# Performance work log

Measured on AMD Instinct MI355X. Metric: run time of the kernel, lower is better.

The kernel has to match this reference:

```python
import jax, jax.numpy as jnp
import numpy as np

NEG_SLOPE = 0.2


def _gat_layer(x, W, a_src, a_dst, src, dst, ew, num_nodes):
    # Dense projection: [N, Din] @ [Din, Dout] -> [N, Dout]
    h = x @ W
    s = h @ a_src  # per-node source score, [N]
    d = h @ a_dst  # per-node destination score, [N]
    score = jax.nn.leaky_relu(s[src] + d[dst], NEG_SLOPE)  # [E]
    # segment softmax over incoming edges of each destination node
    m = jax.ops.segment_max(score, dst, num_segments=num_nodes)
    ex = jnp.exp(score - m[dst])
    denom = jax.ops.segment_sum(ex, dst, num_segments=num_nodes)
    alpha = ex / jnp.maximum(denom[dst], jnp.asarray(1e-16, ex.dtype))
    alpha = alpha * ew  # edge-weighted attention
    # gather h_j, scale by alpha, scatter-add into destinations
    return jax.ops.segment_sum(h[src] * alpha[:, None], dst, num_segments=num_nodes)


def setup_inputs() -> dict:
    key = jax.random.key(0)
    ks = jax.random.split(key, 9)
    N, E, F_IN, HID, NC = 100000, 1600000, 256, 64, 40
    x = jax.random.normal(ks[0], (N, F_IN), dtype=jnp.float32)
    edge_index = jax.random.randint(ks[1], (2, E), 0, N, dtype=jnp.int32)
    edge_weight = jax.random.uniform(ks[2], (E,), dtype=jnp.float32)
    W1 = jax.random.normal(ks[3], (F_IN, HID), dtype=jnp.float32) / np.sqrt(F_IN)
    a1_src = jax.random.normal(ks[4], (HID,), dtype=jnp.float32) / np.sqrt(HID)
    a1_dst = jax.random.normal(ks[5], (HID,), dtype=jnp.float32) / np.sqrt(HID)
    W2 = jax.random.normal(ks[6], (HID, NC), dtype=jnp.float32) / np.sqrt(HID)
    a2_src = jax.random.normal(ks[7], (NC,), dtype=jnp.float32) / np.sqrt(NC)
    a2_dst = jax.random.normal(ks[8], (NC,), dtype=jnp.float32) / np.sqrt(NC)
    return {"x": x, "edge_index": edge_index, "edge_weight": edge_weight,
            "W1": W1, "a1_src": a1_src, "a1_dst": a1_dst,
            "W2": W2, "a2_src": a2_src, "a2_dst": a2_dst}


def reference(x, edge_index, edge_weight, W1, a1_src, a1_dst, W2, a2_src, a2_dst):
    N = x.shape[0]
    # add_self_loops=True in both convs: append (i, i) edges with weight 1
    loops = jnp.arange(N, dtype=edge_index.dtype)
    src = jnp.concatenate([edge_index[0], loops])
    dst = jnp.concatenate([edge_index[1], loops])
    ew = jnp.concatenate([edge_weight, jnp.ones((N,), edge_weight.dtype)])
    h = jax.nn.relu(_gat_layer(x, W1, a1_src, a1_dst, src, dst, ew, N))
    # dropout inactive in eval mode
    out = _gat_layer(h, W2, a2_src, a2_dst, src, dst, ew, N)
    return out
```

## Files before the change

### kernel.cpp

```cpp
#include <hip/hip_runtime.h>
#include <hip/hip_bf16.h>
#include <math.h>

#define NEG_SLOPE 0.2f

typedef __attribute__((ext_vector_type(4))) float f32x4;
typedef __attribute__((ext_vector_type(8))) short bf16x8;
typedef __attribute__((ext_vector_type(4))) short bf16x4;

__device__ __forceinline__ float leaky(float x) { return x > 0.f ? x : NEG_SLOPE * x; }

__device__ __forceinline__ unsigned short bf_hi(float x) {
  return (unsigned short)(__float_as_uint(x) >> 16);
}

__device__ __forceinline__ unsigned short bf_rne(float x) {
  unsigned u = __float_as_uint(x);
  return (unsigned short)((u + 0x7FFFu + ((u >> 16) & 1u)) >> 16);
}


#define BIN_CHUNK 2048
#define BCAP 8192

__global__ void k_curinit(int* __restrict__ cursor, int NB) {
  int i = blockIdx.x * blockDim.x + threadIdx.x;
  if (i < NB) cursor[i] = i * BCAP;
}

__global__ __launch_bounds__(256)
void k_bin(const int* __restrict__ ei, const float* __restrict__ ew, int E, int N,
           int* __restrict__ cursor, int2* __restrict__ staged, int NB) {
  __shared__ int lhist[512];
  __shared__ int lbase[512];
  int tid = threadIdx.x;
  int start = blockIdx.x * BIN_CHUNK;
  int NT = E + N;
  int srcv[8], dstv[8]; float wv[8];
#pragma unroll
  for (int j = 0; j < 8; j++) {
    int e = start + j * 256 + tid;
    int s = 0, d = -1; float w = 0.f;
    if (e < NT) {
      if (e < E) { s = ei[e]; d = ei[E + e]; w = ew[e]; }
      else       { s = d = e - E; w = 1.f; }
    }
    srcv[j] = s; dstv[j] = d; wv[j] = w;
  }
  for (int b = tid; b < NB; b += 256) lhist[b] = 0;
  __syncthreads();
#pragma unroll
  for (int j = 0; j < 8; j++)
    if (dstv[j] >= 0) atomicAdd(&lhist[dstv[j] >> 8], 1);
  __syncthreads();
  for (int b = tid; b < NB; b += 256) {
    int n = lhist[b];
    lbase[b] = (n > 0) ? atomicAdd(&cursor[b], n) : 0;
    lhist[b] = 0;
  }
  __syncthreads();
#pragma unroll
  for (int j = 0; j < 8; j++) {
    if (dstv[j] >= 0) {
      int bkt = dstv[j] >> 8;
      int off = atomicAdd(&lhist[bkt], 1);
      staged[lbase[bkt] + off] =
          make_int2(srcv[j] | ((dstv[j] & 255) << 24), __float_as_int(wv[j]));
    }
  }
}

__global__ __launch_bounds__(512)
void k_bscan(const int* __restrict__ cursor, int NB, int NT, int N,
             int* __restrict__ bbase, int* __restrict__ rp) {
  __shared__ int sm[512];
  int tid = threadIdx.x;
  int v = (tid < NB) ? cursor[tid] - tid * BCAP : 0;
  sm[tid] = v;
  __syncthreads();
  for (int off = 1; off < 512; off <<= 1) {
    int x = sm[tid];
    int a = (tid >= off) ? sm[tid - off] : 0;
    __syncthreads();
    sm[tid] = x + a;
    __syncthreads();
  }
  if (tid < NB) bbase[tid] = sm[tid] - v;
  if (tid == 0) { bbase[NB] = sm[NB - 1]; rp[N] = NT; }
}

__global__ __launch_bounds__(512)
void k_finalize(const int2* __restrict__ staged, const int* __restrict__ bbase,
                int N, int* __restrict__ rp, int2* __restrict__ csr) {
  __shared__ int cnt[256];
  __shared__ int sm[256];
  int b = blockIdx.x, tid = threadIdx.x;
  int sbase = b * BCAP;
  int cbase = bbase[b];
  int size = bbase[b + 1] - cbase;
  if (tid < 256) cnt[tid] = 0;
  __syncthreads();
  for (int i = tid; i < size; i += 512) {
    int2 v = staged[sbase + i];
    atomicAdd(&cnt[((unsigned)v.x) >> 24], 1);
  }
  __syncthreads();
  int s = 0;
  if (tid < 256) { s = cnt[tid]; sm[tid] = s; }
  __syncthreads();
  for (int off = 1; off < 256; off <<= 1) {
    int x = 0;
    if (tid < 256) { x = sm[tid]; if (tid >= off) x += sm[tid - off]; }
    __syncthreads();
    if (tid < 256) sm[tid] = x;
    __syncthreads();
  }
  if (tid < 256) {
    int excl = sm[tid] - s;
    int node = (b << 8) + tid;
    if (node < N) rp[node] = cbase + excl;
    cnt[tid] = excl;
  }
  __syncthreads();
  for (int i = tid; i < size; i += 512) {
    int2 v = staged[sbase + i];
    int dlow = ((unsigned)v.x) >> 24;
    int pos = cbase + atomicAdd(&cnt[dlow], 1);
    csr[pos] = make_int2(v.x & 0x00FFFFFF, v.y);
  }
}

__global__ __launch_bounds__(256)
void k_wprep(const float* __restrict__ W, int K, int Mout,
             unsigned short* __restrict__ whi, unsigned short* __restrict__ wlo) {
  int idx = blockIdx.x * 256 + threadIdx.x;
  if (idx >= K * 64) return;
  int k = idx >> 6, n = idx & 63;
  float v = (n < Mout) ? W[(size_t)k * Mout + n] : 0.f;
  unsigned short h = bf_hi(v);
  float hf = __uint_as_float((unsigned)h << 16);
  unsigned short l = bf_hi(v - hf);
  int kc = k >> 5, kk = k & 31, quad = kk >> 3, j = kk & 7;
  int ct = n >> 4, nn = n & 15;
  int off = (((kc * 4 + ct) * 64) + quad * 16 + nn) * 8 + j;
  whi[off] = h; wlo[off] = l;
}

__global__ __launch_bounds__(256)
void k_gemm_mfma(const float* __restrict__ X, int K,
                 const unsigned short* __restrict__ WHI, const unsigned short* __restrict__ WLO,
                 const float* __restrict__ ASRC, const float* __restrict__ ADST, int Mout,
                 float* __restrict__ Hf, unsigned short* __restrict__ Hb, int ldH,
                 float* __restrict__ S, float* __restrict__ D, int N) {
  __shared__ __align__(16) unsigned short xhi[2048], xlo[2048];
  __shared__ __align__(16) unsigned short whs[2048], wls[2048];
  int tid = threadIdx.x;
  int lane = tid & 63, w = tid >> 6;
  int rowBase = blockIdx.x * 64;

  f32x4 acc[4];
#pragma unroll
  for (int c = 0; c < 4; c++) acc[c] = (f32x4){0.f, 0.f, 0.f, 0.f};

  int q0 = tid, q1 = tid + 256;
  int row0 = q0 >> 3, k40 = (q0 & 7) << 2;
  int row1 = q1 >> 3, k41 = (q1 & 7) << 2;
  int xo0 = (((row0 >> 4) * 64) + (k40 >> 3) * 16 + (row0 & 15)) * 8 + (k40 & 7);
  int xo1 = (((row1 >> 4) * 64) + (k41 >> 3) * 16 + (row1 & 15)) * 8 + (k41 & 7);
  int grow0 = rowBase + row0, grow1 = rowBase + row1;

  int nch = K >> 5;
  f32x4 xr0, xr1; bf16x8 wh, wl;

  xr0 = (f32x4){0.f, 0.f, 0.f, 0.f}; xr1 = xr0;
  if (grow0 < N) xr0 = *(const f32x4*)&X[(size_t)grow0 * K + k40];
  if (grow1 < N) xr1 = *(const f32x4*)&X[(size_t)grow1 * K + k41];
  wh = *(const bf16x8*)(WHI + tid * 8);
  wl = *(const bf16x8*)(WLO + tid * 8);

  for (int kc = 0; kc < nch; kc++) {
    bf16x4 h4, l4;
#pragma unroll
    for (int i = 0; i < 4; i++) {
      unsigned short h = bf_hi(xr0[i]);
      float hf = __uint_as_float((unsigned)h << 16);
      h4[i] = (short)h; l4[i] = (short)bf_hi(xr0[i] - hf);
    }
    *(bf16x4*)(xhi + xo0) = h4; *(bf16x4*)(xlo + xo0) = l4;
#pragma unroll
    for (int i = 0; i < 4; i++) {
      unsigned short h = bf_hi(xr1[i]);
      float hf = __uint_as_float((unsigned)h << 16);
      h4[i] = (short)h; l4[i] = (short)bf_hi(xr1[i] - hf);
    }
    *(bf16x4*)(xhi + xo1) = h4; *(bf16x4*)(xlo + xo1) = l4;
    *(bf16x8*)(whs + tid * 8) = wh;
    *(bf16x8*)(wls + tid * 8) = wl;
    __syncthreads();

    if (kc + 1 < nch) {
      int kb = (kc + 1) << 5;
      xr0 = (f32x4){0.f, 0.f, 0.f, 0.f}; xr1 = xr0;
      if (grow0 < N) xr0 = *(const f32x4*)&X[(size_t)grow0 * K + kb + k40];
      if (grow1 < N) xr1 = *(const f32x4*)&X[(size_t)grow1 * K + kb + k41];
      wh = *(const bf16x8*)(WHI + (size_t)(kc + 1) * 2048 + tid * 8);
      wl = *(const bf16x8*)(WLO + (size_t)(kc + 1) * 2048 + tid * 8);
    }

    bf16x8 ah = *(const bf16x8*)(xhi + (w * 64 + lane) * 8);
    bf16x8 al = *(const bf16x8*)(xlo + (w * 64 + lane) * 8);
#pragma unroll
    for (int c = 0; c < 4; c++) {
      bf16x8 bh = *(const bf16x8*)(whs + (c * 64 + lane) * 8);
      bf16x8 bl = *(const bf16x8*)(wls + (c * 64 + lane) * 8);
      acc[c] = __builtin_amdgcn_mfma_f32_16x16x32_bf16(ah, bh, acc[c], 0, 0, 0);
      acc[c] = __builtin_amdgcn_mfma_f32_16x16x32_bf16(ah, bl, acc[c], 0, 0, 0);
      acc[c] = __builtin_amdgcn_mfma_f32_16x16x32_bf16(al, bh, acc[c], 0, 0, 0);
    }
    __syncthreads();
  }

  int nn = lane & 15, quad = lane >> 4;
  float as_[4], ad_[4];
#pragma unroll
  for (int c = 0; c < 4; c++) {
    int col = c * 16 + nn;
    as_[c] = (col < Mout) ? ASRC[col] : 0.f;
    ad_[c] = (col < Mout) ? ADST[col] : 0.f;
  }
#pragma unroll
  for (int r = 0; r < 4; r++) {
    int grow = rowBase + w * 16 + quad * 4 + r;
    float ps = 0.f, pd = 0.f;
#pragma unroll
    for (int c = 0; c < 4; c++) {
      float v = acc[c][r];
      int col = c * 16 + nn;
      if (grow < N && col < Mout) {
        if (Hb) Hb[(size_t)grow * ldH + col] = bf_rne(v);
        else    Hf[(size_t)grow * ldH + col] = v;
      }
      ps += v * as_[c]; pd += v * ad_[c];
    }
#pragma unroll
    for (int off = 1; off < 16; off <<= 1) {
      ps += __shfl_xor(ps, off);
      pd += __shfl_xor(pd, off);
    }
    if (nn == 0 && grow < N) { S[grow] = ps; D[grow] = pd; }
  }
}

__global__ __launch_bounds__(256)
void k_coef(const int* __restrict__ rp, const int2* __restrict__ csr,
            const float* __restrict__ S, const float* __restrict__ D,
            int2* __restrict__ ec, int N) {
  int gw = (blockIdx.x * blockDim.x + threadIdx.x) >> 6;
  int lane = threadIdx.x & 63;
  int sub = lane >> 4, fl = lane & 15;
  int node = gw * 4 + sub;
  int b = 0, e = 0; float dd = 0.f;
  if (node < N) { b = rp[node]; e = rp[node + 1]; dd = D[node]; }
  float m = -1e30f, den = 0.f;
  for (int t = b; t < e; t += 16) {
    int i = t + fl;
    bool v = i < e;
    int2 p = csr[v ? i : e - 1];
    float c = v ? leaky(S[p.x] + dd) : -1e30f;
    float bm = c;
    bm = fmaxf(bm, __shfl_xor(bm, 1));
    bm = fmaxf(bm, __shfl_xor(bm, 2));
    bm = fmaxf(bm, __shfl_xor(bm, 4));
    bm = fmaxf(bm, __shfl_xor(bm, 8));
    bm = fmaxf(bm, m);
    float r = __expf(m - bm);
    float ex = v ? __expf(c - bm) : 0.f;
    ex += __shfl_xor(ex, 1);
    ex += __shfl_xor(ex, 2);
    ex += __shfl_xor(ex, 4);
    ex += __shfl_xor(ex, 8);
    den = den * r + ex;
    m = bm;
  }
  float inv = 1.f / fmaxf(den, 1e-16f);
  for (int t = b; t < e; t += 16) {
    int i = t + fl;
    if (i < e) {
      int2 p = csr[i];
      float c = leaky(S[p.x] + dd);
      float coef = __expf(c - m) * __int_as_float(p.y) * inv;
      ec[i] = make_int2(p.x, __float_as_int(coef));
    }
  }
}

template <bool BF16>
__global__ __launch_bounds__(256)
void k_agg_fused(const int* __restrict__ rp, const int2* __restrict__ ec,
                 const void* __restrict__ HinV, int ldh,
                 float* __restrict__ Out, int F4, int ldo, int do_relu, int N) {
  int gw = (blockIdx.x * blockDim.x + threadIdx.x) >> 6;
  int lane = threadIdx.x & 63;
  int sub = lane >> 4, fl = lane & 15;
  int node = gw * 4 + sub;
  bool active = node < N;
  bool fless = fl < F4;
  int b = 0, e = 1;
  if (active) { b = rp[node]; e = rp[node + 1]; }
  f32x4 acc0 = (f32x4){0.f, 0.f, 0.f, 0.f};
  f32x4 acc1 = (f32x4){0.f, 0.f, 0.f, 0.f};

  int need = e - b;
  need = max(need, __shfl_xor(need, 16));
  need = max(need, __shfl_xor(need, 32));
  int iters = (need + 7) >> 3;
  int last = e - 1;

  int t = b;
  for (int it = 0; it < iters; it++, t += 8) {
    int idx[8]; float cf[8]; f32x4 hv[8];
#pragma unroll
    for (int j = 0; j < 8; j++) {
      int tj = t + j < e ? t + j : last;
      int2 p = ec[tj];
      idx[j] = p.x;
      cf[j] = (t + j < e) ? __int_as_float(p.y) : 0.f;
    }
#pragma unroll
    for (int j = 0; j < 8; j++) {
      hv[j] = (f32x4){0.f, 0.f, 0.f, 0.f};
      if (fless) {
        if (BF16) {
          const unsigned short* Hb = (const unsigned short*)HinV;
          ushort4 uv = *(const ushort4*)(Hb + (size_t)idx[j] * ldh + (fl << 2));
          hv[j][0] = __uint_as_float((unsigned)uv.x << 16);
          hv[j][1] = __uint_as_float((unsigned)uv.y << 16);
          hv[j][2] = __uint_as_float((unsigned)uv.z << 16);
          hv[j][3] = __uint_as_float((unsigned)uv.w << 16);
        } else {
          const float* Hf = (const float*)HinV;
          hv[j] = *(const f32x4*)&Hf[(size_t)idx[j] * ldh + (fl << 2)];
        }
      }
    }
#pragma unroll
    for (int j = 0; j < 8; j += 2) {
      acc0 += hv[j] * cf[j];
      acc1 += hv[j + 1] * cf[j + 1];
    }
  }

  if (active && fless) {
    f32x4 o = acc0 + acc1;
    if (do_relu) {
#pragma unroll
      for (int j = 0; j < 4; j++) o[j] = fmaxf(o[j], 0.f);
    }
    *(f32x4*)&Out[(size_t)node * ldo + (fl << 2)] = o;
  }
}

extern "C" void kernel_launch(void* const* d_in, const int* in_sizes, int n_in,
                              void* d_out, int out_size, void* d_ws, size_t ws_size,
                              hipStream_t stream) {
  const float* x   = (const float*)d_in[0];
  const int*   ei  = (const int*)d_in[1];
  const float* ew  = (const float*)d_in[2];
  const float* W1  = (const float*)d_in[3];
  const float* a1s = (const float*)d_in[4];
  const float* a1d = (const float*)d_in[5];
  const float* W2  = (const float*)d_in[6];
  const float* a2s = (const float*)d_in[7];
  const float* a2d = (const float*)d_in[8];

  const int HID = in_sizes[4];
  const int NC  = in_sizes[7];
  const int FIN = in_sizes[3] / HID;
  const int N   = in_sizes[0] / FIN;
  const int E   = in_sizes[2];
  const int NT  = E + N;
  const int NB  = (N + 255) >> 8;
  float* out = (float*)d_out;

  char* wsb = (char*)d_ws;
  size_t off = 0;
  auto alloc = [&](size_t bytes) -> char* {
    char* p = wsb + off;
    off += (bytes + 255) & ~(size_t)255;
    return p;
  };
  unsigned short* h1b = (unsigned short*)alloc((size_t)N * 64 * 2);
  float* h2     = (float*)alloc((size_t)N * 64 * 4);
  float* g2     = (float*)alloc((size_t)N * 40 * 4);
  float* S      = (float*)alloc((size_t)N * 4);
  float* D      = (float*)alloc((size_t)N * 4);
  int*   rp     = (int*)alloc((size_t)(N + 1) * 4);
  int*   bbase  = (int*)alloc((size_t)(NB + 1) * 4);
  int*   cursor = (int*)alloc((size_t)NB * 4);
  int2*  csr    = (int2*)alloc((size_t)NT * 8);
  int2*  staged = (int2*)alloc((size_t)NB * BCAP * 8);
  unsigned short* whi1 = (unsigned short*)alloc((size_t)FIN * 64 * 2);
  unsigned short* wlo1 = (unsigned short*)alloc((size_t)FIN * 64 * 2);
  unsigned short* whi2 = (unsigned short*)alloc((size_t)HID * 64 * 2);
  unsigned short* wlo2 = (unsigned short*)alloc((size_t)HID * 64 * 2);
  int2* ec = staged;
  (void)ws_size; (void)n_in; (void)out_size;

  const int ebins = (NT + BIN_CHUNK - 1) / BIN_CHUNK;

  hipLaunchKernelGGL(k_curinit, dim3((NB + 255) / 256), dim3(256), 0, stream, cursor, NB);
  hipLaunchKernelGGL(k_bin, dim3(ebins), dim3(256), 0, stream, ei, ew, E, N, cursor, staged, NB);
  hipLaunchKernelGGL(k_bscan, dim3(1), dim3(512), 0, stream, cursor, NB, NT, N, bbase, rp);
  hipLaunchKernelGGL(k_finalize, dim3(NB), dim3(512), 0, stream, staged, bbase, N, rp, csr);

  hipLaunchKernelGGL(k_wprep, dim3((FIN * 64 + 255) / 256), dim3(256), 0, stream,
                     W1, FIN, HID, whi1, wlo1);
  hipLaunchKernelGGL(k_wprep, dim3((HID * 64 + 255) / 256), dim3(256), 0, stream,
                     W2, HID, NC, whi2, wlo2);

  const int gblocks = (N + 63) / 64;
  const int ablocks = (N + 15) / 16;

  hipLaunchKernelGGL(k_gemm_mfma, dim3(gblocks), dim3(256), 0, stream,
                     x, FIN, whi1, wlo1, a1s, a1d, HID, (float*)nullptr, h1b, 64, S, D, N);
  hipLaunchKernelGGL(k_coef, dim3(ablocks), dim3(256), 0, stream, rp, csr, S, D, ec, N);
  hipLaunchKernelGGL((k_agg_fused<true>), dim3(ablocks), dim3(256), 0, stream,
                     rp, ec, (const void*)h1b, 64, h2, 16, 64, 1, N);

  hipLaunchKernelGGL(k_gemm_mfma, dim3(gblocks), dim3(256), 0, stream,
                     h2, HID, whi2, wlo2, a2s, a2d, NC, g2, (unsigned short*)nullptr, 40, S, D, N);
  hipLaunchKernelGGL(k_coef, dim3(ablocks), dim3(256), 0, stream, rp, csr, S, D, ec, N);
  hipLaunchKernelGGL((k_agg_fused<false>), dim3(ablocks), dim3(256), 0, stream,
                     rp, ec, (const void*)g2, 40, out, 10, NC, 0, N);
}
```

Measured before the change: 402.9 us.

## Fuse softmax coefficient computation into aggregation with online softmax

Removes the separate k_coef kernel and computes the attention coefficients inside the aggregation kernel, using an online softmax that rescales the running accumulators whenever the running max grows. This avoids a second pass over the CSR edges and the write and re-read of the ec coefficient array. Every feature lane of a node now recomputes the leaky-relu scores and exponentials redundantly and gathers S per edge, and the normalisation moves to the end. The g2 row stride is also padded from 40 to 48 floats so rows stay aligned for the vector loads.

```diff
diff --git a/kernel.cpp b/kernel.cpp
--- a/kernel.cpp
+++ b/kernel.cpp
@@ -251,52 +251,10 @@
   }
 }
 
-__global__ __launch_bounds__(256)
-void k_coef(const int* __restrict__ rp, const int2* __restrict__ csr,
-            const float* __restrict__ S, const float* __restrict__ D,
-            int2* __restrict__ ec, int N) {
-  int gw = (blockIdx.x * blockDim.x + threadIdx.x) >> 6;
-  int lane = threadIdx.x & 63;
-  int sub = lane >> 4, fl = lane & 15;
-  int node = gw * 4 + sub;
-  int b = 0, e = 0; float dd = 0.f;
-  if (node < N) { b = rp[node]; e = rp[node + 1]; dd = D[node]; }
-  float m = -1e30f, den = 0.f;
-  for (int t = b; t < e; t += 16) {
-    int i = t + fl;
-    bool v = i < e;
-    int2 p = csr[v ? i : e - 1];
-    float c = v ? leaky(S[p.x] + dd) : -1e30f;
-    float bm = c;
-    bm = fmaxf(bm, __shfl_xor(bm, 1));
-    bm = fmaxf(bm, __shfl_xor(bm, 2));
-    bm = fmaxf(bm, __shfl_xor(bm, 4));
-    bm = fmaxf(bm, __shfl_xor(bm, 8));
-    bm = fmaxf(bm, m);
-    float r = __expf(m - bm);
-    float ex = v ? __expf(c - bm) : 0.f;
-    ex += __shfl_xor(ex, 1);
-    ex += __shfl_xor(ex, 2);
-    ex += __shfl_xor(ex, 4);
-    ex += __shfl_xor(ex, 8);
-    den = den * r + ex;
-    m = bm;
-  }
-  float inv = 1.f / fmaxf(den, 1e-16f);
-  for (int t = b; t < e; t += 16) {
-    int i = t + fl;
-    if (i < e) {
-      int2 p = csr[i];
-      float c = leaky(S[p.x] + dd);
-      float coef = __expf(c - m) * __int_as_float(p.y) * inv;
-      ec[i] = make_int2(p.x, __float_as_int(coef));
-    }
-  }
-}
-
 template <bool BF16>
 __global__ __launch_bounds__(256)
-void k_agg_fused(const int* __restrict__ rp, const int2* __restrict__ ec,
+void k_agg_fused(const int* __restrict__ rp, const int2* __restrict__ csr,
+                 const float* __restrict__ S, const float* __restrict__ D,
                  const void* __restrict__ HinV, int ldh,
                  float* __restrict__ Out, int F4, int ldo, int do_relu, int N) {
   int gw = (blockIdx.x * blockDim.x + threadIdx.x) >> 6;
@@ -305,8 +263,9 @@
   int node = gw * 4 + sub;
   bool active = node < N;
   bool fless = fl < F4;
-  int b = 0, e = 1;
-  if (active) { b = rp[node]; e = rp[node + 1]; }
+  int b = 0, e = 1; float dd = 0.f;
+  if (active) { b = rp[node]; e = rp[node + 1]; dd = D[node]; }
+  float m = -1e30f, den = 0.f;
   f32x4 acc0 = (f32x4){0.f, 0.f, 0.f, 0.f};
   f32x4 acc1 = (f32x4){0.f, 0.f, 0.f, 0.f};
 
@@ -318,14 +277,16 @@
 
   int t = b;
   for (int it = 0; it < iters; it++, t += 8) {
-    int idx[8]; float cf[8]; f32x4 hv[8];
+    int  idx[8]; float wgt[8], sv[8], cc[8], ex[8]; f32x4 hv[8];
 #pragma unroll
     for (int j = 0; j < 8; j++) {
       int tj = t + j < e ? t + j : last;
-      int2 p = ec[tj];
+      int2 p = csr[tj];
       idx[j] = p.x;
-      cf[j] = (t + j < e) ? __int_as_float(p.y) : 0.f;
-    }
+      wgt[j] = (t + j < e) ? __int_as_float(p.y) : 0.f;
+    }
+#pragma unroll
+    for (int j = 0; j < 8; j++) sv[j] = S[idx[j]];
 #pragma unroll
     for (int j = 0; j < 8; j++) {
       hv[j] = (f32x4){0.f, 0.f, 0.f, 0.f};
@@ -344,14 +305,27 @@
       }
     }
 #pragma unroll
-    for (int j = 0; j < 8; j += 2) {
-      acc0 += hv[j] * cf[j];
-      acc1 += hv[j + 1] * cf[j + 1];
-    }
+    for (int j = 0; j < 8; j++) cc[j] = (t + j < e) ? leaky(sv[j] + dd) : -1e30f;
+    float bm = m;
+#pragma unroll
+    for (int j = 0; j < 8; j++) bm = fmaxf(bm, cc[j]);
+    if (bm > m) {
+      float r = __expf(m - bm);
+      den *= r; acc0 *= r; acc1 *= r;
+      m = bm;
+    }
+#pragma unroll
+    for (int j = 0; j < 8; j++) ex[j] = (t + j < e) ? __expf(cc[j] - m) : 0.f;
+    den += ((ex[0] + ex[1]) + (ex[2] + ex[3])) + ((ex[4] + ex[5]) + (ex[6] + ex[7]));
+    acc0 += hv[0] * (ex[0] * wgt[0]) + hv[1] * (ex[1] * wgt[1])
+          + hv[2] * (ex[2] * wgt[2]) + hv[3] * (ex[3] * wgt[3]);
+    acc1 += hv[4] * (ex[4] * wgt[4]) + hv[5] * (ex[5] * wgt[5])
+          + hv[6] * (ex[6] * wgt[6]) + hv[7] * (ex[7] * wgt[7]);
   }
 
   if (active && fless) {
-    f32x4 o = acc0 + acc1;
+    float inv = 1.0f / fmaxf(den, 1e-16f);
+    f32x4 o = (acc0 + acc1) * inv;
     if (do_relu) {
 #pragma unroll
       for (int j = 0; j < 4; j++) o[j] = fmaxf(o[j], 0.f);
@@ -391,7 +365,7 @@
   };
   unsigned short* h1b = (unsigned short*)alloc((size_t)N * 64 * 2);
   float* h2     = (float*)alloc((size_t)N * 64 * 4);
-  float* g2     = (float*)alloc((size_t)N * 40 * 4);
+  float* g2     = (float*)alloc((size_t)N * 48 * 4);
   float* S      = (float*)alloc((size_t)N * 4);
   float* D      = (float*)alloc((size_t)N * 4);
   int*   rp     = (int*)alloc((size_t)(N + 1) * 4);
@@ -403,7 +377,6 @@
   unsigned short* wlo1 = (unsigned short*)alloc((size_t)FIN * 64 * 2);
   unsigned short* whi2 = (unsigned short*)alloc((size_t)HID * 64 * 2);
   unsigned short* wlo2 = (unsigned short*)alloc((size_t)HID * 64 * 2);
-  int2* ec = staged;
   (void)ws_size; (void)n_in; (void)out_size;
 
   const int ebins = (NT + BIN_CHUNK - 1) / BIN_CHUNK;
@@ -423,13 +396,11 @@
 
   hipLaunchKernelGGL(k_gemm_mfma, dim3(gblocks), dim3(256), 0, stream,
                      x, FIN, whi1, wlo1, a1s, a1d, HID, (float*)nullptr, h1b, 64, S, D, N);
-  hipLaunchKernelGGL(k_coef, dim3(ablocks), dim3(256), 0, stream, rp, csr, S, D, ec, N);
   hipLaunchKernelGGL((k_agg_fused<true>), dim3(ablocks), dim3(256), 0, stream,
-                     rp, ec, (const void*)h1b, 64, h2, 16, 64, 1, N);
+                     rp, csr, S, D, (const void*)h1b, 64, h2, 16, 64, 1, N);
 
   hipLaunchKernelGGL(k_gemm_mfma, dim3(gblocks), dim3(256), 0, stream,
-                     h2, HID, whi2, wlo2, a2s, a2d, NC, g2, (unsigned short*)nullptr, 40, S, D, N);
-  hipLaunchKernelGGL(k_coef, dim3(ablocks), dim3(256), 0, stream, rp, csr, S, D, ec, N);
+                     h2, HID, whi2, wlo2, a2s, a2d, NC, g2, (unsigned short*)nullptr, 48, S, D, N);
   hipLaunchKernelGGL((k_agg_fused<false>), dim3(ablocks), dim3(256), 0, stream,
-                     rp, ec, (const void*)g2, 40, out, 10, NC, 0, N);
-}
+                     rp, csr, S, D, (const void*)g2, 48, out, 10, NC, 0, N);
+}
```

New measurement: 379.9 us. 1.06x faster.
